# Performance work log

Hardware: AMD Instinct MI355X
Metric: run time of the kernel (lower is better)

The kernel has to match this reference:

```python
import jax, jax.numpy as jnp
from jax import lax
import numpy as np

C = 256
RATE = 4
NUM_HEADS = 4
WS = 8
EPS = 1e-5


def setup_inputs() -> dict:
    key = jax.random.key(0)
    ks = jax.random.split(key, 24)
    cr = C // RATE  # 64
    s = 0.02
    return {
        "x": jax.random.normal(ks[0], (32, C, 64, 64), jnp.float32),
        # qkv / out projections (stored as [in, out] for x @ W)
        "qkv_w": jax.random.normal(ks[1], (C, 3 * C), jnp.float32) * s,
        "qkv_b": jnp.zeros((3 * C,), jnp.float32),
        "out_w": jax.random.normal(ks[2], (C, C), jnp.float32) * s,
        "out_b": jnp.zeros((C,), jnp.float32),
        # channel-attention MLP
        "ca_w1": jax.random.normal(ks[3], (C, cr), jnp.float32) * s,
        "ca_b1": jnp.zeros((cr,), jnp.float32),
        "ca_w2": jax.random.normal(ks[4], (cr, C), jnp.float32) * s,
        "ca_b2": jnp.zeros((C,), jnp.float32),
        # spatial attention: Conv2d(C, cr, 7, pad=3, groups=cr) -> OIHW (cr, C//cr, 7, 7)
        "sa_w1": jax.random.normal(ks[5], (cr, C // cr, 7, 7), jnp.float32) * s,
        "sa_b1": jnp.zeros((cr,), jnp.float32),
        "bn1_g": jnp.ones((cr,), jnp.float32),
        "bn1_b": jnp.zeros((cr,), jnp.float32),
        "bn1_m": jnp.zeros((cr,), jnp.float32),
        "bn1_v": jnp.ones((cr,), jnp.float32),
        # Conv2d(cr, C, 7, pad=3, groups=cr) -> OIHW (C, 1, 7, 7)
        "sa_w2": jax.random.normal(ks[6], (C, 1, 7, 7), jnp.float32) * s,
        "sa_b2": jnp.zeros((C,), jnp.float32),
        "bn2_g": jnp.ones((C,), jnp.float32),
        "bn2_b": jnp.zeros((C,), jnp.float32),
        "bn2_m": jnp.zeros((C,), jnp.float32),
        "bn2_v": jnp.ones((C,), jnp.float32),
    }


def _bn(y, g, b, m, v):
    # inference-mode BatchNorm2d over channel axis 1
    inv = g / jnp.sqrt(v + EPS)
    return y * inv[None, :, None, None] + (b - m * inv)[None, :, None, None]


def reference(x, qkv_w, qkv_b, out_w, out_b, ca_w1, ca_b1, ca_w2, ca_b2,
              sa_w1, sa_b1, bn1_g, bn1_b, bn1_m, bn1_v,
              sa_w2, sa_b2, bn2_g, bn2_b, bn2_m, bn2_v):
    b, c, h, w = x.shape
    hd = c // NUM_HEADS
    # ---- channel attention gating ----
    xp = x.transpose(0, 2, 3, 1)                      # b,h,w,c
    a = jax.nn.relu(xp @ ca_w1 + ca_b1) @ ca_w2 + ca_b2
    x = x * jax.nn.sigmoid(a.transpose(0, 3, 1, 2))   # b,c,h,w
    # ---- windowed multi-head self-attention ----
    nwh, nww = h // WS, w // WS
    xw = x.reshape(b, c, nwh, WS, nww, WS).transpose(0, 2, 4, 3, 5, 1)
    xw = xw.reshape(-1, WS * WS, c)                   # (b*nwin, 64, c)
    qkv = xw @ qkv_w + qkv_b
    q, k, v = jnp.split(qkv, 3, axis=-1)
    def heads(t):
        return t.reshape(-1, WS * WS, NUM_HEADS, hd).transpose(0, 2, 1, 3)
    q, k, v = heads(q), heads(k), heads(v)            # (nw, H, 64, hd)
    attn = jax.nn.softmax(jnp.einsum('whqd,whkd->whqk', q, k) * (hd ** -0.5), axis=-1)
    o = jnp.einsum('whqk,whkd->whqd', attn, v).transpose(0, 2, 1, 3).reshape(-1, WS * WS, c)
    o = o @ out_w + out_b
    o = o.reshape(b, nwh, nww, WS, WS, c).transpose(0, 5, 1, 3, 2, 4).reshape(b, c, h, w)
    x = x + o
    # ---- channel shuffle (groups=4) ----
    g = 4
    x = x.reshape(b, g, c // g, h, w).transpose(0, 2, 1, 3, 4).reshape(b, c, h, w)
    # ---- spatial attention branch ----
    dn = ('NCHW', 'OIHW', 'NCHW')
    cr = c // RATE
    y = lax.conv_general_dilated(x, sa_w1, (1, 1), [(3, 3), (3, 3)],
                                 dimension_numbers=dn, feature_group_count=cr)
    y = _bn(y + sa_b1[None, :, None, None], bn1_g, bn1_b, bn1_m, bn1_v)
    y = jax.nn.relu(y)
    y = lax.conv_general_dilated(y, sa_w2, (1, 1), [(3, 3), (3, 3)],
                                 dimension_numbers=dn, feature_group_count=cr)
    y = _bn(y + sa_b2[None, :, None, None], bn2_g, bn2_b, bn2_m, bn2_v)
    return x * jax.nn.sigmoid(y)
```

## Files before the change

### kernel.cpp

```cpp
#include <hip/hip_runtime.h>

#define HW 4096
#define CCH 256

typedef __bf16 bf16x8 __attribute__((ext_vector_type(8)));
typedef float f32x4 __attribute__((ext_vector_type(4)));
typedef float f32x2 __attribute__((ext_vector_type(2)));
typedef unsigned u32x2 __attribute__((ext_vector_type(2)));
typedef unsigned short u16;

#define SWZ8(r) ((((r) + ((r) >> 2)) & 7) << 3)

__device__ __forceinline__ u16 f2b(float f) {
  union { __bf16 h; u16 u; } c; c.h = (__bf16)f; return c.u;
}
__device__ __forceinline__ unsigned f2b2(float a, float b) {
  union { __bf16 h[2]; unsigned u; } c;
  c.h[0] = (__bf16)a; c.h[1] = (__bf16)b; return c.u;
}
__device__ __forceinline__ float b2f(u16 h) {
  union { unsigned u; float f; } v; v.u = ((unsigned)h) << 16; return v.f;
}
__device__ __forceinline__ void nt_store4(const float4& v, float* p) {
  f32x4 t; t[0] = v.x; t[1] = v.y; t[2] = v.z; t[3] = v.w;
  __builtin_nontemporal_store(t, reinterpret_cast<f32x4*>(p));
}

__global__ __launch_bounds__(256) void kprep(
    const float* __restrict__ qkv_w, const float* __restrict__ out_w,
    const float* __restrict__ ca_w1, const float* __restrict__ ca_w2,
    u16* __restrict__ wq2, u16* __restrict__ wo2,
    u16* __restrict__ c1f, u16* __restrict__ c2f)
{
  int i = blockIdx.x * 256 + threadIdx.x;
  int j = i & 7, lane = (i >> 3) & 63, l15 = lane & 15, lg = lane >> 4;
  if (i < 48 * 8 * 512) {
    int kb = (i >> 9) & 7, T = i >> 12;
    wq2[i] = f2b(qkv_w[(kb * 32 + lg * 8 + j) * 768 + T * 16 + l15]);
  }
  if (i < 16 * 8 * 512) {
    int kb = (i >> 9) & 7, T = i >> 12;
    wo2[i] = f2b(out_w[(kb * 32 + lg * 8 + j) * 256 + T * 16 + l15]);
  }
  if (i < 4 * 8 * 512) {
    int kb = (i >> 9) & 7, T = i >> 12;
    c1f[i] = f2b(ca_w1[(kb * 32 + lg * 8 + j) * 64 + T * 16 + l15]);
  }
  if (i < 16 * 2 * 512) {
    int kb = (i >> 9) & 1, T = i >> 10;
    c2f[i] = f2b(ca_w2[(kb * 32 + lg * 8 + j) * 256 + T * 16 + l15]);
  }
}

__global__ __launch_bounds__(256, 4) void kb_attn(
    const float* __restrict__ x, u16* __restrict__ x2w, u16* __restrict__ Og,
    const u16* __restrict__ wq2, const float* __restrict__ qkv_b,
    const float* __restrict__ out_b,
    const u16* __restrict__ c1f, const float* __restrict__ ca_b1,
    const u16* __restrict__ c2f, const float* __restrict__ ca_b2)
{
  __shared__ u16 smem[20480];
  u16* pX  = smem;
  u16* pH  = smem + 16384;
  u16* pQ  = smem;
  u16* pK  = smem + 4096;
  u16* pVT = smem + 8192;

  const int tid = threadIdx.x;
  const int lane = tid & 63;
  const int wv = __builtin_amdgcn_readfirstlane(tid >> 6);
  const int l15 = lane & 15;
  const int lg = lane >> 4;

  const int bid = blockIdx.x;
  const int wid = (bid & 7) * 256 + (bid >> 3);
  const int b = wid >> 6, wrem = wid & 63;
  const int pbase = (wrem >> 3) * (8 * 64) + (wrem & 7) * 8;
  const float* ximg = x + (size_t)b * CCH * HW;

  const int tokA = wv * 16 + l15;
  const int swA = SWZ8(tokA);

  {
    const int t0 = l15 * 4;
    const int prow = pbase + (l15 >> 1) * 64 + (l15 & 1) * 4;
    #pragma unroll 2
    for (int i = 0; i < 16; ++i) {
      int c = i * 16 + wv * 4 + lg;
      const float4 v = *reinterpret_cast<const float4*>(&ximg[(size_t)c * HW + prow]);
      pX[(t0 + 0) * 256 + (c ^ SWZ8(t0 + 0))] = f2b(v.x);
      pX[(t0 + 1) * 256 + (c ^ SWZ8(t0 + 1))] = f2b(v.y);
      pX[(t0 + 2) * 256 + (c ^ SWZ8(t0 + 2))] = f2b(v.z);
      pX[(t0 + 3) * 256 + (c ^ SWZ8(t0 + 3))] = f2b(v.w);
    }
  }
  __syncthreads();

  uint2 gpk[16];
  {
    bf16x8 aXr[8];
    #pragma unroll
    for (int kb = 0; kb < 8; ++kb)
      aXr[kb] = *reinterpret_cast<const bf16x8*>(&pX[tokA * 256 + ((kb * 32 + lg * 8) ^ swA)]);
    #pragma unroll
    for (int nt1 = 0; nt1 < 4; ++nt1) {
      f32x4 c1 = {0.f, 0.f, 0.f, 0.f};
      #pragma unroll
      for (int kb = 0; kb < 8; ++kb) {
        bf16x8 bw = *reinterpret_cast<const bf16x8*>(&c1f[(nt1 * 8 + kb) * 512 + lane * 8]);
        c1 = __builtin_amdgcn_mfma_f32_16x16x32_bf16(aXr[kb], bw, c1, 0, 0, 0);
      }
      float bias1 = ca_b1[nt1 * 16 + l15];
      #pragma unroll
      for (int r = 0; r < 4; ++r) {
        int tok = wv * 16 + lg * 4 + r;
        pH[tok * 64 + ((nt1 * 16 + l15) ^ SWZ8(tok))] = f2b(fmaxf(c1[r] + bias1, 0.f));
      }
    }
    bf16x8 hB[2];
    #pragma unroll
    for (int kb = 0; kb < 2; ++kb)
      hB[kb] = *reinterpret_cast<const bf16x8*>(&pH[tokA * 64 + ((kb * 32 + lg * 8) ^ swA)]);
    #pragma unroll
    for (int nt = 0; nt < 16; ++nt) {
      f32x4 a2 = {0.f, 0.f, 0.f, 0.f};
      #pragma unroll
      for (int kb = 0; kb < 2; ++kb) {
        bf16x8 w2a = *reinterpret_cast<const bf16x8*>(&c2f[(nt * 2 + kb) * 512 + lane * 8]);
        a2 = __builtin_amdgcn_mfma_f32_16x16x32_bf16(w2a, hB[kb], a2, 0, 0, 0);
      }
      const int n0 = nt * 16 + lg * 4;
      const ushort4 xq = *reinterpret_cast<const ushort4*>(&pX[tokA * 256 + (n0 ^ swA)]);
      float xg0 = b2f(xq.x) / (1.f + __expf(-(a2[0] + ca_b2[n0])));
      float xg1 = b2f(xq.y) / (1.f + __expf(-(a2[1] + ca_b2[n0 + 1])));
      float xg2 = b2f(xq.z) / (1.f + __expf(-(a2[2] + ca_b2[n0 + 2])));
      float xg3 = b2f(xq.w) / (1.f + __expf(-(a2[3] + ca_b2[n0 + 3])));
      uint2 pk;
      pk.x = f2b2(xg0, xg1);
      pk.y = f2b2(xg2, xg3);
      gpk[nt] = pk;
      *reinterpret_cast<uint2*>(&pX[tokA * 256 + (n0 ^ swA)]) = pk;
    }
  }

  {
    u16* wout = x2w + (size_t)wid * 16384;
    #pragma unroll
    for (int nt0 = 0; nt0 < 4; ++nt0) {
      #pragma unroll
      for (int r = 0; r < 4; ++r) {
        int cq = nt0 * 16 + lg * 4 + r;
        unsigned v0 = (r < 2) ? (gpk[nt0     ].x >> (16 * r)) : (gpk[nt0     ].y >> (16 * (r - 2)));
        unsigned v1 = (r < 2) ? (gpk[nt0 +  4].x >> (16 * r)) : (gpk[nt0 +  4].y >> (16 * (r - 2)));
        unsigned v2 = (r < 2) ? (gpk[nt0 +  8].x >> (16 * r)) : (gpk[nt0 +  8].y >> (16 * (r - 2)));
        unsigned v3 = (r < 2) ? (gpk[nt0 + 12].x >> (16 * r)) : (gpk[nt0 + 12].y >> (16 * (r - 2)));
        u32x2 o;
        o[0] = f2b2(b2f((u16)v0) + out_b[cq],       b2f((u16)v1) + out_b[cq + 64]);
        o[1] = f2b2(b2f((u16)v2) + out_b[cq + 128], b2f((u16)v3) + out_b[cq + 192]);
        __builtin_nontemporal_store(o, reinterpret_cast<u32x2*>(&wout[cq * 256 + tokA * 4]));
      }
    }
  }

  bf16x8 aG[8];
  #pragma unroll
  for (int kb = 0; kb < 8; ++kb)
    aG[kb] = *reinterpret_cast<const bf16x8*>(&pX[tokA * 256 + ((kb * 32 + lg * 8) ^ swA)]);
  __syncthreads();

  u16* ogw = Og + (size_t)wid * 16384;

  for (int h = 0; h < 4; ++h) {
    #pragma unroll 2
    for (int tau = 0; tau < 12; ++tau) {
      int kind = tau >> 2, sub = tau & 3;
      int colbase = kind * 256 + h * 64 + sub * 16;
      int T = kind * 16 + h * 4 + sub;
      f32x4 acc = {0.f, 0.f, 0.f, 0.f};
      #pragma unroll
      for (int kb = 0; kb < 8; ++kb) {
        bf16x8 bw = *reinterpret_cast<const bf16x8*>(&wq2[(T * 8 + kb) * 512 + lane * 8]);
        acc = __builtin_amdgcn_mfma_f32_16x16x32_bf16(aG[kb], bw, acc, 0, 0, 0);
      }
      float bias = qkv_b[colbase + l15];
      #pragma unroll
      for (int r = 0; r < 4; ++r) {
        int tok = wv * 16 + lg * 4 + r;
        u16 uv = f2b(acc[r] + bias);
        int d = sub * 16 + l15;
        if (kind == 0)      pQ [tok * 64 + (d ^ SWZ8(tok))] = uv;
        else if (kind == 1) pK [tok * 64 + (d ^ SWZ8(tok))] = uv;
        else                pVT[d * 64 + (tok ^ ((d & 7) << 3))] = uv;
      }
    }
    __syncthreads();

    bf16x8 aQ[2];
    #pragma unroll
    for (int kb = 0; kb < 2; ++kb)
      aQ[kb] = *reinterpret_cast<const bf16x8*>(&pQ[tokA * 64 + ((kb * 32 + lg * 8) ^ swA)]);
    f32x4 s4[4];
    #pragma unroll
    for (int jt = 0; jt < 4; ++jt) {
      int krow = jt * 16 + l15;
      int swk = SWZ8(krow);
      f32x4 acc = {0.f, 0.f, 0.f, 0.f};
      #pragma unroll
      for (int kb = 0; kb < 2; ++kb) {
        bf16x8 bK = *reinterpret_cast<const bf16x8*>(&pK[krow * 64 + ((kb * 32 + lg * 8) ^ swk)]);
        acc = __builtin_amdgcn_mfma_f32_16x16x32_bf16(aQ[kb], bK, acc, 0, 0, 0);
      }
      s4[jt] = acc;
    }
    #pragma unroll
    for (int r = 0; r < 4; ++r) {
      float m = fmaxf(fmaxf(s4[0][r], s4[1][r]), fmaxf(s4[2][r], s4[3][r]));
      #pragma unroll
      for (int off = 1; off < 16; off <<= 1) m = fmaxf(m, __shfl_xor(m, off));
      float e0 = __expf((s4[0][r] - m) * 0.125f);
      float e1 = __expf((s4[1][r] - m) * 0.125f);
      float e2 = __expf((s4[2][r] - m) * 0.125f);
      float e3 = __expf((s4[3][r] - m) * 0.125f);
      float sum = e0 + e1 + e2 + e3;
      #pragma unroll
      for (int off = 1; off < 16; off <<= 1) sum += __shfl_xor(sum, off);
      float is = 1.f / sum;
      int tok = wv * 16 + lg * 4 + r;
      int swp = SWZ8(tok);
      pQ[tok * 64 + ((     l15) ^ swp)] = f2b(e0 * is);
      pQ[tok * 64 + ((16 + l15) ^ swp)] = f2b(e1 * is);
      pQ[tok * 64 + ((32 + l15) ^ swp)] = f2b(e2 * is);
      pQ[tok * 64 + ((48 + l15) ^ swp)] = f2b(e3 * is);
    }
    bf16x8 bP[2];
    #pragma unroll
    for (int kb = 0; kb < 2; ++kb)
      bP[kb] = *reinterpret_cast<const bf16x8*>(&pQ[tokA * 64 + ((kb * 32 + lg * 8) ^ swA)]);
    #pragma unroll
    for (int dt = 0; dt < 4; ++dt) {
      int drow = dt * 16 + l15;
      int swd = (drow & 7) << 3;
      f32x4 acc = {0.f, 0.f, 0.f, 0.f};
      #pragma unroll
      for (int kb = 0; kb < 2; ++kb) {
        bf16x8 aV = *reinterpret_cast<const bf16x8*>(&pVT[drow * 64 + ((kb * 32 + lg * 8) ^ swd)]);
        acc = __builtin_amdgcn_mfma_f32_16x16x32_bf16(aV, bP[kb], acc, 0, 0, 0);
      }
      int d0 = h * 64 + dt * 16 + lg * 4;
      uint2 pk;
      pk.x = f2b2(acc[0], acc[1]);
      pk.y = f2b2(acc[2], acc[3]);
      *reinterpret_cast<uint2*>(&ogw[(d0 >> 2) * 256 + tokA * 4]) = pk;
    }
    __syncthreads();
  }
}

__global__ __launch_bounds__(256, 3) void kb_oproj(
    const u16* __restrict__ Og, const u16* __restrict__ wo2,
    u16* __restrict__ x2w)
{
  const int tid = threadIdx.x;
  const int lane = tid & 63;
  const int wv = __builtin_amdgcn_readfirstlane(tid >> 6);
  const int l15 = lane & 15;
  const int lg = lane >> 4;
  const int bid = blockIdx.x;
  const int wid = (bid & 7) * 256 + (bid >> 3);
  const int tokA = wv * 16 + l15;

  const u16* og = Og + (size_t)wid * 16384;
  bf16x8 bO[8];
  #pragma unroll
  for (int kb = 0; kb < 8; ++kb) {
    int dq = kb * 8 + lg * 2;
    uint2 lo = *reinterpret_cast<const uint2*>(&og[dq * 256 + tokA * 4]);
    uint2 hi = *reinterpret_cast<const uint2*>(&og[(dq + 1) * 256 + tokA * 4]);
    union { uint4 u; bf16x8 v; } cvt;
    cvt.u.x = lo.x; cvt.u.y = lo.y; cvt.u.z = hi.x; cvt.u.w = hi.y;
    bO[kb] = cvt.v;
  }

  f32x4 acc[16];
  #pragma unroll
  for (int nt = 0; nt < 16; ++nt) {
    f32x4 z = {0.f, 0.f, 0.f, 0.f};
    acc[nt] = z;
  }
  #pragma unroll
  for (int nt = 0; nt < 16; ++nt) {
    #pragma unroll
    for (int kb = 0; kb < 8; ++kb) {
      bf16x8 wA = *reinterpret_cast<const bf16x8*>(&wo2[(nt * 8 + kb) * 512 + lane * 8]);
      acc[nt] = __builtin_amdgcn_mfma_f32_16x16x32_bf16(wA, bO[kb], acc[nt], 0, 0, 0);
    }
  }

  u16* wout = x2w + (size_t)wid * 16384;
  #pragma unroll
  for (int nt0 = 0; nt0 < 4; ++nt0) {
    #pragma unroll
    for (int r = 0; r < 4; ++r) {
      int cq = nt0 * 16 + lg * 4 + r;
      u16* p = &wout[cq * 256 + tokA * 4];
      uint2 cur = *reinterpret_cast<const uint2*>(p);
      float c0 = b2f((u16)(cur.x & 0xffff)) + acc[nt0     ][r];
      float c1 = b2f((u16)(cur.x >> 16))    + acc[nt0 +  4][r];
      float c2 = b2f((u16)(cur.y & 0xffff)) + acc[nt0 +  8][r];
      float c3 = b2f((u16)(cur.y >> 16))    + acc[nt0 + 12][r];
      uint2 o;
      o.x = f2b2(c0, c1);
      o.y = f2b2(c2, c3);
      *reinterpret_cast<uint2*>(p) = o;
    }
  }
}

__global__ __launch_bounds__(256) void kc_conv1(
    const u16* __restrict__ x2w, const float* __restrict__ w1, const float* __restrict__ b1,
    const float* __restrict__ g1, const float* __restrict__ bb1,
    const float* __restrict__ m1, const float* __restrict__ v1,
    float* __restrict__ y1)
{
  __shared__ float sin_[4 * 22 * 72];
  const int bid = blockIdx.x;
  const int wid = (bid & 7) * 1024 + (bid >> 3);
  int b = wid >> 8, rem = wid & 255, j = rem >> 2, qt = rem & 3;
  const u16* xw = x2w + (size_t)b * 64 * 16384;
  for (int idx = threadIdx.x; idx < 22 * 70; idx += 256) {
    int yy = idx / 70, xx = idx - yy * 70;
    int ih = qt * 16 + yy - 3, iw = xx - 3;
    uint2 v = {0u, 0u};
    if (ih >= 0 && ih < 64 && iw >= 0 && iw < 64) {
      int wr = (ih >> 3) * 8 + (iw >> 3);
      int tok = (ih & 7) * 8 + (iw & 7);
      v = *reinterpret_cast<const uint2*>(&xw[(size_t)wr * 16384 + j * 256 + tok * 4]);
    }
    sin_[0 * 1584 + yy * 72 + xx] = b2f((u16)(v.x & 0xffff));
    sin_[1 * 1584 + yy * 72 + xx] = b2f((u16)(v.x >> 16));
    sin_[2 * 1584 + yy * 72 + xx] = b2f((u16)(v.y & 0xffff));
    sin_[3 * 1584 + yy * 72 + xx] = b2f((u16)(v.y >> 16));
  }
  __syncthreads();

  float inv = g1[j] / sqrtf(v1[j] + 1e-5f);
  float shf = bb1[j] - m1[j] * inv;
  float bia = b1[j];
  float* yo = y1 + ((size_t)b * 64 + j) * HW + qt * 16 * 64;
  const float* wbase = w1 + j * 4 * 49;

  int y = threadIdx.x >> 4, x4 = (threadIdx.x & 15) * 4;
  float a0 = 0.f, a1 = 0.f, a2 = 0.f, a3 = 0.f;
  for (int i = 0; i < 4; ++i) {
    #pragma unroll
    for (int ky = 0; ky < 7; ++ky) {
      const float* row = sin_ + (i * 22 + y + ky) * 72 + x4;
      const f32x4 p0 = *reinterpret_cast<const f32x4*>(row);
      const f32x4 p1 = *reinterpret_cast<const f32x4*>(row + 4);
      const f32x2 p2 = *reinterpret_cast<const f32x2*>(row + 8);
      float v[10] = {p0[0], p0[1], p0[2], p0[3], p1[0], p1[1], p1[2], p1[3], p2[0], p2[1]};
      const float* wr = wbase + (i * 7 + ky) * 7;
      #pragma unroll
      for (int kx = 0; kx < 7; ++kx) {
        float wvv = wr[kx];
        a0 += v[kx] * wvv; a1 += v[kx+1] * wvv;
        a2 += v[kx+2] * wvv; a3 += v[kx+3] * wvv;
      }
    }
  }
  float4 r4;
  r4.x = fmaxf((a0 + bia) * inv + shf, 0.f);
  r4.y = fmaxf((a1 + bia) * inv + shf, 0.f);
  r4.z = fmaxf((a2 + bia) * inv + shf, 0.f);
  r4.w = fmaxf((a3 + bia) * inv + shf, 0.f);
  nt_store4(r4, yo + y * 64 + x4);
}

__global__ __launch_bounds__(256) void kd_conv2(
    const float* __restrict__ y1, const u16* __restrict__ x2w,
    const float* __restrict__ w2, const float* __restrict__ b2,
    const float* __restrict__ g2, const float* __restrict__ bb2,
    const float* __restrict__ m2, const float* __restrict__ v2,
    float* __restrict__ out)
{
  __shared__ float sin_[70 * 72];
  const int bid = blockIdx.x;
  const int wid = (bid & 7) * 256 + (bid >> 3);
  int b = wid >> 6, g = wid & 63;
  const float* yin = y1 + ((size_t)b * 64 + g) * HW;

  for (int idx = threadIdx.x; idx < 6 * 72; idx += 256) {
    int r = idx / 72, c = idx - r * 72;
    sin_[(r < 3 ? r : 64 + r) * 72 + c] = 0.f;
  }
  for (int idx = threadIdx.x; idx < 64 * 6; idx += 256) {
    int r = idx / 6, c = idx - r * 6;
    sin_[(r + 3) * 72 + (c < 3 ? c : 64 + c)] = 0.f;
  }
  for (int idx = threadIdx.x; idx < 64 * 16; idx += 256) {
    int r = idx >> 4, c4 = (idx & 15) * 4;
    const float4 v = *reinterpret_cast<const float4*>(&yin[r * 64 + c4]);
    float* d = &sin_[(r + 3) * 72 + 3 + c4];
    d[0] = v.x; d[1] = v.y; d[2] = v.z; d[3] = v.w;
  }
  __syncthreads();

  float inv[4], shf[4], bia[4];
  #pragma unroll
  for (int i = 0; i < 4; ++i) {
    int n = 4 * g + i;
    float sc = g2[n] / sqrtf(v2[n] + 1e-5f);
    inv[i] = sc; shf[i] = bb2[n] - m2[n] * sc; bia[i] = b2[n];
  }
  const float* wb = w2 + 4 * g * 49;
  const u16* xw = x2w + (size_t)b * 64 * 16384;

  for (int it = 0; it < 4; ++it) {
    int s = it * 256 + threadIdx.x;
    int y = s >> 4, x4 = (s & 15) * 4;
    float acc[4][4] = {};
    #pragma unroll
    for (int ky = 0; ky < 7; ++ky) {
      const float* row = sin_ + (y + ky) * 72 + x4;
      const f32x4 p0 = *reinterpret_cast<const f32x4*>(row);
      const f32x4 p1 = *reinterpret_cast<const f32x4*>(row + 4);
      const f32x2 p2 = *reinterpret_cast<const f32x2*>(row + 8);
      float v[10] = {p0[0], p0[1], p0[2], p0[3], p1[0], p1[1], p1[2], p1[3], p2[0], p2[1]};
      #pragma unroll
      for (int i = 0; i < 4; ++i) {
        const float* wr = wb + i * 49 + ky * 7;
        #pragma unroll
        for (int kx = 0; kx < 7; ++kx) {
          float wvv = wr[kx];
          acc[i][0] += v[kx] * wvv; acc[i][1] += v[kx+1] * wvv;
          acc[i][2] += v[kx+2] * wvv; acc[i][3] += v[kx+3] * wvv;
        }
      }
    }
    int po = y * 64 + x4;
    int wr_ = (y >> 3) * 8 + (x4 >> 3);
    int t0 = (y & 7) * 8 + (x4 & 7);
    const u16* gp = &xw[(size_t)wr_ * 16384 + g * 256 + t0 * 4];
    uint2 q0 = *reinterpret_cast<const uint2*>(gp + 0);
    uint2 q1 = *reinterpret_cast<const uint2*>(gp + 4);
    uint2 q2 = *reinterpret_cast<const uint2*>(gp + 8);
    uint2 q3 = *reinterpret_cast<const uint2*>(gp + 12);
    #pragma unroll
    for (int i = 0; i < 4; ++i) {
      int n = 4 * g + i;
      float* op = out + ((size_t)b * 256 + n) * HW + po;
      float y0 = (acc[i][0] + bia[i]) * inv[i] + shf[i];
      float y1v = (acc[i][1] + bia[i]) * inv[i] + shf[i];
      float y2 = (acc[i][2] + bia[i]) * inv[i] + shf[i];
      float y3 = (acc[i][3] + bia[i]) * inv[i] + shf[i];
      float g0 = b2f((u16)(i < 2 ? (q0.x >> (16 * i)) : (q0.y >> (16 * (i - 2)))));
      float g1v = b2f((u16)(i < 2 ? (q1.x >> (16 * i)) : (q1.y >> (16 * (i - 2)))));
      float g2v = b2f((u16)(i < 2 ? (q2.x >> (16 * i)) : (q2.y >> (16 * (i - 2)))));
      float g3 = b2f((u16)(i < 2 ? (q3.x >> (16 * i)) : (q3.y >> (16 * (i - 2)))));
      float4 r;
      r.x = g0  / (1.f + __expf(-y0));
      r.y = g1v / (1.f + __expf(-y1v));
      r.z = g2v / (1.f + __expf(-y2));
      r.w = g3  / (1.f + __expf(-y3));
      nt_store4(r, op);
    }
  }
}

extern "C" void kernel_launch(void* const* d_in, const int* in_sizes, int n_in,
                              void* d_out, int out_size, void* d_ws, size_t ws_size,
                              hipStream_t stream) {
  const float* x     = (const float*)d_in[0];
  const float* qkv_w = (const float*)d_in[1];
  const float* qkv_b = (const float*)d_in[2];
  const float* out_w = (const float*)d_in[3];
  const float* out_b = (const float*)d_in[4];
  const float* ca_w1 = (const float*)d_in[5];
  const float* ca_b1 = (const float*)d_in[6];
  const float* ca_w2 = (const float*)d_in[7];
  const float* ca_b2 = (const float*)d_in[8];
  const float* sa_w1 = (const float*)d_in[9];
  const float* sa_b1 = (const float*)d_in[10];
  const float* bn1_g = (const float*)d_in[11];
  const float* bn1_b = (const float*)d_in[12];
  const float* bn1_m = (const float*)d_in[13];
  const float* bn1_v = (const float*)d_in[14];
  const float* sa_w2 = (const float*)d_in[15];
  const float* sa_b2 = (const float*)d_in[16];
  const float* bn2_g = (const float*)d_in[17];
  const float* bn2_b = (const float*)d_in[18];
  const float* bn2_m = (const float*)d_in[19];
  const float* bn2_v = (const float*)d_in[20];

  float* outp = (float*)d_out;
  u16* x2w = (u16*)d_ws;
  float* y1 = (float*)(x2w + (size_t)2048 * 16384);

  u16* wq2 = (u16*)d_out;
  u16* wo2 = wq2 + 48 * 8 * 512;
  u16* c1f = wo2 + 16 * 8 * 512;
  u16* c2f = c1f + 4 * 8 * 512;
  u16* Og  = c2f + 16 * 2 * 512;

  kprep   <<<768,  256, 0, stream>>>(qkv_w, out_w, ca_w1, ca_w2, wq2, wo2, c1f, c2f);
  kb_attn <<<2048, 256, 0, stream>>>(x, x2w, Og, wq2, qkv_b, out_b, c1f, ca_b1, c2f, ca_b2);
  kb_oproj<<<2048, 256, 0, stream>>>(Og, wo2, x2w);
  kc_conv1<<<8192, 256, 0, stream>>>(x2w, sa_w1, sa_b1, bn1_g, bn1_b, bn1_m, bn1_v, y1);
  kd_conv2<<<2048, 256, 0, stream>>>(y1, x2w, sa_w2, sa_b2, bn2_g, bn2_b, bn2_m, bn2_v, outp);
}
```

Baseline: 441.4 us.

## Store conv1 intermediate in bf16 and pack attention LDS stores via transposed MFMA

Conv1 now writes its ReLU output as bf16 instead of fp32, and conv2 unpacks it, halving the intermediate's global traffic. In the attention kernel the MFMA operands are swapped so each lane owns four consecutive columns. This lets the channel-MLP hidden, Q and K tiles be written with packed 8-byte LDS stores and the biases loaded as float4. The cost is an extra bf16 rounding of the spatial-attention intermediate, which adds some precision loss.

```diff
diff --git a/kernel.cpp b/kernel.cpp
--- a/kernel.cpp
+++ b/kernel.cpp
@@ -108,14 +108,14 @@
       #pragma unroll
       for (int kb = 0; kb < 8; ++kb) {
         bf16x8 bw = *reinterpret_cast<const bf16x8*>(&c1f[(nt1 * 8 + kb) * 512 + lane * 8]);
-        c1 = __builtin_amdgcn_mfma_f32_16x16x32_bf16(aXr[kb], bw, c1, 0, 0, 0);
-      }
-      float bias1 = ca_b1[nt1 * 16 + l15];
-      #pragma unroll
-      for (int r = 0; r < 4; ++r) {
-        int tok = wv * 16 + lg * 4 + r;
-        pH[tok * 64 + ((nt1 * 16 + l15) ^ SWZ8(tok))] = f2b(fmaxf(c1[r] + bias1, 0.f));
-      }
+        c1 = __builtin_amdgcn_mfma_f32_16x16x32_bf16(bw, aXr[kb], c1, 0, 0, 0);
+      }
+      const float4 b14 = *reinterpret_cast<const float4*>(&ca_b1[nt1 * 16 + lg * 4]);
+      uint2 pk;
+      pk.x = f2b2(fmaxf(c1[0] + b14.x, 0.f), fmaxf(c1[1] + b14.y, 0.f));
+      pk.y = f2b2(fmaxf(c1[2] + b14.z, 0.f), fmaxf(c1[3] + b14.w, 0.f));
+      int d0 = nt1 * 16 + lg * 4;
+      *reinterpret_cast<uint2*>(&pH[tokA * 64 + (d0 ^ swA)]) = pk;
     }
     bf16x8 hB[2];
     #pragma unroll
@@ -130,11 +130,12 @@
         a2 = __builtin_amdgcn_mfma_f32_16x16x32_bf16(w2a, hB[kb], a2, 0, 0, 0);
       }
       const int n0 = nt * 16 + lg * 4;
+      const float4 b24 = *reinterpret_cast<const float4*>(&ca_b2[n0]);
       const ushort4 xq = *reinterpret_cast<const ushort4*>(&pX[tokA * 256 + (n0 ^ swA)]);
-      float xg0 = b2f(xq.x) / (1.f + __expf(-(a2[0] + ca_b2[n0])));
-      float xg1 = b2f(xq.y) / (1.f + __expf(-(a2[1] + ca_b2[n0 + 1])));
-      float xg2 = b2f(xq.z) / (1.f + __expf(-(a2[2] + ca_b2[n0 + 2])));
-      float xg3 = b2f(xq.w) / (1.f + __expf(-(a2[3] + ca_b2[n0 + 3])));
+      float xg0 = b2f(xq.x) / (1.f + __expf(-(a2[0] + b24.x)));
+      float xg1 = b2f(xq.y) / (1.f + __expf(-(a2[1] + b24.y)));
+      float xg2 = b2f(xq.z) / (1.f + __expf(-(a2[2] + b24.z)));
+      float xg3 = b2f(xq.w) / (1.f + __expf(-(a2[3] + b24.w)));
       uint2 pk;
       pk.x = f2b2(xg0, xg1);
       pk.y = f2b2(xg2, xg3);
@@ -180,17 +181,23 @@
       #pragma unroll
       for (int kb = 0; kb < 8; ++kb) {
         bf16x8 bw = *reinterpret_cast<const bf16x8*>(&wq2[(T * 8 + kb) * 512 + lane * 8]);
-        acc = __builtin_amdgcn_mfma_f32_16x16x32_bf16(aG[kb], bw, acc, 0, 0, 0);
-      }
-      float bias = qkv_b[colbase + l15];
-      #pragma unroll
-      for (int r = 0; r < 4; ++r) {
-        int tok = wv * 16 + lg * 4 + r;
-        u16 uv = f2b(acc[r] + bias);
-        int d = sub * 16 + l15;
-        if (kind == 0)      pQ [tok * 64 + (d ^ SWZ8(tok))] = uv;
-        else if (kind == 1) pK [tok * 64 + (d ^ SWZ8(tok))] = uv;
-        else                pVT[d * 64 + (tok ^ ((d & 7) << 3))] = uv;
+        acc = __builtin_amdgcn_mfma_f32_16x16x32_bf16(bw, aG[kb], acc, 0, 0, 0);
+      }
+      const float4 bia4 = *reinterpret_cast<const float4*>(&qkv_b[colbase + lg * 4]);
+      if (kind == 2) {
+        #pragma unroll
+        for (int r = 0; r < 4; ++r) {
+          int d = sub * 16 + lg * 4 + r;
+          float bv = (r == 0) ? bia4.x : (r == 1) ? bia4.y : (r == 2) ? bia4.z : bia4.w;
+          pVT[d * 64 + (tokA ^ ((d & 7) << 3))] = f2b(acc[r] + bv);
+        }
+      } else {
+        uint2 pk;
+        pk.x = f2b2(acc[0] + bia4.x, acc[1] + bia4.y);
+        pk.y = f2b2(acc[2] + bia4.z, acc[3] + bia4.w);
+        int d0 = sub * 16 + lg * 4;
+        u16* dst = (kind == 0) ? pQ : pK;
+        *reinterpret_cast<uint2*>(&dst[tokA * 64 + (d0 ^ swA)]) = pk;
       }
     }
     __syncthreads();
@@ -320,7 +327,7 @@
     const u16* __restrict__ x2w, const float* __restrict__ w1, const float* __restrict__ b1,
     const float* __restrict__ g1, const float* __restrict__ bb1,
     const float* __restrict__ m1, const float* __restrict__ v1,
-    float* __restrict__ y1)
+    u16* __restrict__ y1)
 {
   __shared__ float sin_[4 * 22 * 72];
   const int bid = blockIdx.x;
@@ -346,7 +353,7 @@
   float inv = g1[j] / sqrtf(v1[j] + 1e-5f);
   float shf = bb1[j] - m1[j] * inv;
   float bia = b1[j];
-  float* yo = y1 + ((size_t)b * 64 + j) * HW + qt * 16 * 64;
+  u16* yo = y1 + ((size_t)b * 64 + j) * HW + qt * 16 * 64;
   const float* wbase = w1 + j * 4 * 49;
 
   int y = threadIdx.x >> 4, x4 = (threadIdx.x & 15) * 4;
@@ -368,16 +375,14 @@
       }
     }
   }
-  float4 r4;
-  r4.x = fmaxf((a0 + bia) * inv + shf, 0.f);
-  r4.y = fmaxf((a1 + bia) * inv + shf, 0.f);
-  r4.z = fmaxf((a2 + bia) * inv + shf, 0.f);
-  r4.w = fmaxf((a3 + bia) * inv + shf, 0.f);
-  nt_store4(r4, yo + y * 64 + x4);
+  u32x2 o;
+  o[0] = f2b2(fmaxf((a0 + bia) * inv + shf, 0.f), fmaxf((a1 + bia) * inv + shf, 0.f));
+  o[1] = f2b2(fmaxf((a2 + bia) * inv + shf, 0.f), fmaxf((a3 + bia) * inv + shf, 0.f));
+  __builtin_nontemporal_store(o, reinterpret_cast<u32x2*>(yo + y * 64 + x4));
 }
 
 __global__ __launch_bounds__(256) void kd_conv2(
-    const float* __restrict__ y1, const u16* __restrict__ x2w,
+    const u16* __restrict__ y1, const u16* __restrict__ x2w,
     const float* __restrict__ w2, const float* __restrict__ b2,
     const float* __restrict__ g2, const float* __restrict__ bb2,
     const float* __restrict__ m2, const float* __restrict__ v2,
@@ -387,7 +392,7 @@
   const int bid = blockIdx.x;
   const int wid = (bid & 7) * 256 + (bid >> 3);
   int b = wid >> 6, g = wid & 63;
-  const float* yin = y1 + ((size_t)b * 64 + g) * HW;
+  const u16* yin = y1 + ((size_t)b * 64 + g) * HW;
 
   for (int idx = threadIdx.x; idx < 6 * 72; idx += 256) {
     int r = idx / 72, c = idx - r * 72;
@@ -399,9 +404,10 @@
   }
   for (int idx = threadIdx.x; idx < 64 * 16; idx += 256) {
     int r = idx >> 4, c4 = (idx & 15) * 4;
-    const float4 v = *reinterpret_cast<const float4*>(&yin[r * 64 + c4]);
+    uint2 v = *reinterpret_cast<const uint2*>(&yin[r * 64 + c4]);
     float* d = &sin_[(r + 3) * 72 + 3 + c4];
-    d[0] = v.x; d[1] = v.y; d[2] = v.z; d[3] = v.w;
+    d[0] = b2f((u16)(v.x & 0xffff)); d[1] = b2f((u16)(v.x >> 16));
+    d[2] = b2f((u16)(v.y & 0xffff)); d[3] = b2f((u16)(v.y >> 16));
   }
   __syncthreads();
 
@@ -494,7 +500,7 @@
 
   float* outp = (float*)d_out;
   u16* x2w = (u16*)d_ws;
-  float* y1 = (float*)(x2w + (size_t)2048 * 16384);
+  u16* y1 = x2w + (size_t)2048 * 16384;
 
   u16* wq2 = (u16*)d_out;
   u16* wo2 = wq2 + 48 * 8 * 512;
```

New measurement: 424.2 us, median of 3. 3.9% less time.
